# Optimization experiments

Hardware: AMD Instinct MI355X
Metric: run time of the kernel (lower is better)

Reference implementation:

```python
import jax, jax.numpy as jnp
import numpy as np

N = 100000      # nodes
E = 1600000     # edges (avg degree 16)
IN = 128        # in_channels
H = 128         # hidden_channels
OUT = 64        # out_channels
NHID = 3        # num_layers (hidden->hidden SAGE convs)


def _lin(k, fan_out, fan_in):
    s = 1.0 / np.sqrt(fan_in)
    return jax.random.uniform(k, (fan_out, fan_in), jnp.float32, -s, s)


def setup_inputs() -> dict:
    key = jax.random.key(0)
    ks = jax.random.split(key, 12)
    x = jax.random.normal(ks[0], (N, IN), dtype=jnp.float32)
    edge_index = jax.random.randint(ks[1], (2, E), 0, N, dtype=jnp.int32)
    # inProj Linear(IN -> H)
    Wp = _lin(ks[2], H, IN)
    bp = jnp.zeros((H,), jnp.float32)
    # 3 hidden SAGEConv(H -> H): lin_l (with bias) on aggregated neighbors, lin_r (no bias) on root
    Wl_h = jnp.stack([_lin(jax.random.fold_in(ks[3], i), H, H) for i in range(NHID)])
    bl_h = jnp.zeros((NHID, H), jnp.float32)
    Wr_h = jnp.stack([_lin(jax.random.fold_in(ks[4], i), H, H) for i in range(NHID)])
    # output SAGEConv(H -> OUT)
    Wl_o = _lin(ks[5], OUT, H)
    bl_o = jnp.zeros((OUT,), jnp.float32)
    Wr_o = _lin(ks[6], OUT, H)
    return {"x": x, "edge_index": edge_index, "Wp": Wp, "bp": bp,
            "Wl_h": Wl_h, "bl_h": bl_h, "Wr_h": Wr_h,
            "Wl_o": Wl_o, "bl_o": bl_o, "Wr_o": Wr_o}


def reference(x, edge_index, Wp, bp, Wl_h, bl_h, Wr_h, Wl_o, bl_o, Wr_o):
    src, dst = edge_index[0], edge_index[1]
    ones = jnp.ones((E,), x.dtype)
    deg = jax.ops.segment_sum(ones, dst, num_segments=N)           # [N]
    inv_deg = (1.0 / jnp.maximum(deg, 1.0))[:, None]               # [N,1]

    def sage(h, Wl, bl, Wr):
        # mean aggregation of source features onto destinations (irregular gather+scatter)
        s = jax.ops.segment_sum(h[src], dst, num_segments=N)       # [N,d]
        mean = s * inv_deg
        return mean @ Wl.T + bl + h @ Wr.T

    h = x @ Wp.T + bp
    inp = h
    h = jax.nn.relu(h)
    for i in range(NHID):
        h = sage(h, Wl_h[i], bl_h[i], Wr_h[i])
        h = jax.nn.relu(h)                                          # dropout is identity in eval
        h = h + 0.2 * inp
    h = sage(h, Wl_o, bl_o, Wr_o)
    return jax.nn.log_softmax(h, axis=-1)
```

## Files before the change

### kernel.cpp

```cpp
#include <hip/hip_runtime.h>
#include <math.h>

#define N_NODES 100000
#define N_EDGES 1600000
#define NBUK 391
#define PCHUNK 8192
#define NPBLK 196
#define AGG_BLOCKS 12504

typedef unsigned short u16;
typedef unsigned char u8;
typedef __bf16 bf16x8 __attribute__((ext_vector_type(8)));
typedef float f32x4 __attribute__((ext_vector_type(4)));
typedef float f32x2 __attribute__((ext_vector_type(2)));

#define OFF_RP      0u
#define OFF_INVDEG  400016u
#define OFF_BHIST   800016u
#define OFF_BBASE   801600u
#define OFF_GCUR    803200u
#define OFF_PCTR    804800u
#define OFF_PAIRS   805056u
#define OFF_COL     13605056u
#define OFF_PACK    20005056u
#define OFF_INP     20267200u
#define OFF_H       45867200u
#define OFF_H8A     71467200u
#define OFF_H8B     84267200u
#define OFF_GL      97067200u
#define OFF_GR      109867200u
#define OFF_MEAN    122667200u
#define WS_NEEDED   148267200u

#define PK_WP   0
#define PK_WL   16384
#define PK_WR   65536
#define PK_WLO  114688
#define PK_WRO  122880

__device__ __forceinline__ float bfl(unsigned u) {
  union { unsigned i; float f; } v; v.i = u << 16; return v.f;
}
__device__ __forceinline__ float bfh(unsigned u) {
  union { unsigned i; float f; } v; v.i = u & 0xFFFF0000u; return v.f;
}
__device__ __forceinline__ u16 f2b(float f) {
  union { float f; unsigned i; } v; v.f = f;
  unsigned r = (v.i + 0x7FFFu + ((v.i >> 16) & 1u)) >> 16;
  return (u16)r;
}

__global__ __launch_bounds__(256) void pack_weights_k(
    const float* __restrict__ Wp, const float* __restrict__ Wl,
    const float* __restrict__ Wr, const float* __restrict__ Wlo,
    const float* __restrict__ Wro, u16* __restrict__ P) {
  int t = blockIdx.x * 256 + threadIdx.x;
  if (t >= 16384) return;
  const float* W; u16* dst; int j; int NT;
  if (t < 2048)        { W = Wp;                    dst = P + PK_WP;                j = t;                 NT = 8; }
  else if (t < 8192)   { int m = (t - 2048) >> 11;  j = (t - 2048) & 2047;
                         W = Wl + (m << 14);        dst = P + PK_WL + (m << 14);    NT = 8; }
  else if (t < 14336)  { int m = (t - 8192) >> 11;  j = (t - 8192) & 2047;
                         W = Wr + (m << 14);        dst = P + PK_WR + (m << 14);    NT = 8; }
  else if (t < 15360)  { j = t - 14336;             W = Wlo;  dst = P + PK_WLO;     NT = 4; }
  else                 { j = t - 15360;             W = Wro;  dst = P + PK_WRO;     NT = 4; }
  int lane = j & 63;
  int nt, kt;
  if (NT == 8) { nt = (j >> 6) & 7; kt = j >> 9; }
  else         { nt = (j >> 6) & 3; kt = j >> 8; }
  int n  = nt * 16 + (lane & 15);
  int k0 = kt * 32 + ((lane >> 4) << 3);
  const float* s = W + n * 128 + k0;
  ushort4 lo = make_ushort4(f2b(s[0]), f2b(s[1]), f2b(s[2]), f2b(s[3]));
  ushort4 hi = make_ushort4(f2b(s[4]), f2b(s[5]), f2b(s[6]), f2b(s[7]));
  *(ushort4*)(dst + j * 8)     = lo;
  *(ushort4*)(dst + j * 8 + 4) = hi;
}

__global__ __launch_bounds__(256) void bhist_k(const int* __restrict__ dst,
                                               int* __restrict__ bhist) {
  __shared__ int lc[NBUK];
  int t = threadIdx.x;
  for (int i = t; i < NBUK; i += 256) lc[i] = 0;
  __syncthreads();
  int base = blockIdx.x * 4096;
#pragma unroll
  for (int r = 0; r < 16; r++) {
    int i = base + r * 256 + t;
    if (i < N_EDGES) atomicAdd(&lc[dst[i] >> 8], 1);
  }
  __syncthreads();
  for (int i = t; i < NBUK; i += 256)
    if (lc[i]) atomicAdd(&bhist[i], lc[i]);
}

__global__ __launch_bounds__(512) void bscan_k(const int* __restrict__ bhist,
                                               int* __restrict__ bbase,
                                               int* __restrict__ gcur,
                                               int* __restrict__ rp) {
  __shared__ int s[512];
  int t = threadIdx.x;
  int v = (t < NBUK) ? bhist[t] : 0;
  s[t] = v;
  __syncthreads();
  for (int off = 1; off < 512; off <<= 1) {
    int u = (t >= off) ? s[t - off] : 0;
    __syncthreads();
    s[t] += u;
    __syncthreads();
  }
  if (t < NBUK) { int e = s[t] - v; bbase[t] = e; gcur[t] = e; }
  if (t == NBUK - 1) { bbase[NBUK] = s[t]; rp[N_NODES] = s[t]; }
}

__global__ __launch_bounds__(256) void part_k(const int* __restrict__ src,
                                              const int* __restrict__ dst,
                                              int* __restrict__ gcur,
                                              uint2* __restrict__ pairs) {
  __shared__ int lcnt[NBUK + 1];
  __shared__ int lofs[512];
  __shared__ int cur[NBUK];
  __shared__ int gslot[NBUK];
  __shared__ uint2 stag[PCHUNK];
  int t = threadIdx.x;
  for (int i = t; i < NBUK + 1; i += 256) lcnt[i] = 0;
  __syncthreads();
  int base = blockIdx.x * PCHUNK;
#pragma unroll
  for (int r = 0; r < PCHUNK / 256; r++) {
    int i = base + r * 256 + t;
    if (i < N_EDGES) atomicAdd(&lcnt[dst[i] >> 8], 1);
  }
  __syncthreads();
  {
    int e1 = t + 256;
    lofs[t]  = (t  <= NBUK) ? lcnt[t]  : 0;
    lofs[e1] = (e1 <= NBUK) ? lcnt[e1] : 0;
    __syncthreads();
    for (int off = 1; off < 512; off <<= 1) {
      int a0 = (t  >= off) ? lofs[t  - off] : 0;
      int a1 = (e1 >= off) ? lofs[e1 - off] : 0;
      __syncthreads();
      lofs[t] += a0; lofs[e1] += a1;
      __syncthreads();
    }
    int o0 = lofs[t]  - ((t  <= NBUK) ? lcnt[t]  : 0);
    int o1 = lofs[e1] - ((e1 <= NBUK) ? lcnt[e1] : 0);
    __syncthreads();
    lofs[t] = o0; lofs[e1] = o1;
    __syncthreads();
  }
  for (int i = t; i < NBUK; i += 256) cur[i] = lofs[i];
  __syncthreads();
#pragma unroll
  for (int r = 0; r < PCHUNK / 256; r++) {
    int i = base + r * 256 + t;
    if (i < N_EDGES) {
      int d = dst[i];
      int slot = atomicAdd(&cur[d >> 8], 1);
      stag[slot] = make_uint2((unsigned)src[i], (unsigned)d);
    }
  }
  __syncthreads();
  for (int i = t; i < NBUK; i += 256)
    if (lcnt[i]) gslot[i] = atomicAdd(&gcur[i], lcnt[i]);
  __syncthreads();
  int total = lofs[NBUK];
  for (int p = t; p < total; p += 256) {
    uint2 pr = stag[p];
    int b = (int)(pr.y >> 8);
    pairs[gslot[b] + (p - lofs[b])] = pr;
  }
}

__global__ __launch_bounds__(256) void csr_k(const uint2* __restrict__ pairs,
                                             const int* __restrict__ bbase,
                                             int* __restrict__ rp,
                                             float* __restrict__ invdeg,
                                             int* __restrict__ col) {
  __shared__ int cnt[256];
  __shared__ int scn[256];
  __shared__ int cur[256];
  int b = blockIdx.x, t = threadIdx.x;
  int lo = bbase[b], hi = bbase[b + 1];
  cnt[t] = 0;
  __syncthreads();
  for (int p = lo + t; p < hi; p += 256)
    atomicAdd(&cnt[pairs[p].y & 255], 1);
  __syncthreads();
  int c = cnt[t];
  scn[t] = c;
  __syncthreads();
  for (int off = 1; off < 256; off <<= 1) {
    int v = (t >= off) ? scn[t - off] : 0;
    __syncthreads();
    scn[t] += v;
    __syncthreads();
  }
  int excl = scn[t] - c;
  int node = (b << 8) + t;
  if (node < N_NODES) {
    rp[node] = lo + excl;
    invdeg[node] = 1.0f / (float)(c > 1 ? c : 1);
  }
  cur[t] = lo + excl;
  __syncthreads();
  for (int p = lo + t; p < hi; p += 256) {
    uint2 pr = pairs[p];
    int slot = atomicAdd(&cur[pr.y & 255], 1);
    col[slot] = (int)pr.x;
  }
}

__global__ __launch_bounds__(256) void aggregate_plane_k(
    const u8* __restrict__ h8, const int* __restrict__ rp,
    const int* __restrict__ col, const float* __restrict__ invdeg,
    u16* __restrict__ mean) {
  int b = blockIdx.x;
  int plane = (b & 7) >> 1;
  int idx = ((b >> 3) << 1) + (b & 1);
  if (idx >= 3125) return;
  int tid = threadIdx.x;
  int grp = tid >> 3, lane8 = tid & 7;
  int node = idx * 32 + grp;
  const u8* hp = h8 + (size_t)plane * (N_NODES * 32) + lane8 * 4;
  u16* mp = mean + (size_t)plane * (N_NODES * 32);
  int beg = rp[node], end = rp[node + 1];
  float a0 = 0.f, a1 = 0.f, a2 = 0.f, a3 = 0.f;
  int j = beg;
  for (; j + 3 < end; j += 4) {
    int s0 = col[j], s1 = col[j + 1], s2 = col[j + 2], s3 = col[j + 3];
    unsigned v0 = *(const unsigned*)(hp + (size_t)s0 * 32);
    unsigned v1 = *(const unsigned*)(hp + (size_t)s1 * 32);
    unsigned v2 = *(const unsigned*)(hp + (size_t)s2 * 32);
    unsigned v3 = *(const unsigned*)(hp + (size_t)s3 * 32);
    f32x2 p0 = __builtin_amdgcn_cvt_pk_f32_fp8(v0, false);
    f32x2 p1 = __builtin_amdgcn_cvt_pk_f32_fp8(v0, true);
    f32x2 p2 = __builtin_amdgcn_cvt_pk_f32_fp8(v1, false);
    f32x2 p3 = __builtin_amdgcn_cvt_pk_f32_fp8(v1, true);
    f32x2 p4 = __builtin_amdgcn_cvt_pk_f32_fp8(v2, false);
    f32x2 p5 = __builtin_amdgcn_cvt_pk_f32_fp8(v2, true);
    f32x2 p6 = __builtin_amdgcn_cvt_pk_f32_fp8(v3, false);
    f32x2 p7 = __builtin_amdgcn_cvt_pk_f32_fp8(v3, true);
    a0 += (p0[0] + p2[0]) + (p4[0] + p6[0]);
    a1 += (p0[1] + p2[1]) + (p4[1] + p6[1]);
    a2 += (p1[0] + p3[0]) + (p5[0] + p7[0]);
    a3 += (p1[1] + p3[1]) + (p5[1] + p7[1]);
  }
  for (; j < end; j++) {
    unsigned v0 = *(const unsigned*)(hp + (size_t)col[j] * 32);
    f32x2 p0 = __builtin_amdgcn_cvt_pk_f32_fp8(v0, false);
    f32x2 p1 = __builtin_amdgcn_cvt_pk_f32_fp8(v0, true);
    a0 += p0[0]; a1 += p0[1]; a2 += p1[0]; a3 += p1[1];
  }
  float wd = invdeg[node];
  *(ushort4*)(mp + (size_t)node * 32 + lane8 * 4) =
      make_ushort4(f2b(a0 * wd), f2b(a1 * wd), f2b(a2 * wd), f2b(a3 * wd));
}

__global__ __launch_bounds__(256) void out_gather_k(
    const u16* __restrict__ gl, const int* __restrict__ rp,
    const int* __restrict__ col, const float* __restrict__ invdeg,
    float* __restrict__ partial) {
  int b = blockIdx.x;
  int plane = (b & 7) >> 1;
  int idx = ((b >> 3) << 1) + (b & 1);
  if (idx >= 3125) return;
  int tid = threadIdx.x;
  int grp = tid >> 3, lane8 = tid & 7;
  int node = idx * 32 + grp;
  const u16* gp = gl + (size_t)plane * (N_NODES * 16) + lane8 * 2;
  int beg = rp[node], end = rp[node + 1];
  float a0 = 0.f, a1 = 0.f;
  int j = beg;
  for (; j + 3 < end; j += 4) {
    int s0 = col[j], s1 = col[j + 1], s2 = col[j + 2], s3 = col[j + 3];
    unsigned v0 = *(const unsigned*)(gp + (size_t)s0 * 16);
    unsigned v1 = *(const unsigned*)(gp + (size_t)s1 * 16);
    unsigned v2 = *(const unsigned*)(gp + (size_t)s2 * 16);
    unsigned v3 = *(const unsigned*)(gp + (size_t)s3 * 16);
    a0 += (bfl(v0) + bfl(v1)) + (bfl(v2) + bfl(v3));
    a1 += (bfh(v0) + bfh(v1)) + (bfh(v2) + bfh(v3));
  }
  for (; j < end; j++) {
    unsigned v0 = *(const unsigned*)(gp + (size_t)col[j] * 16);
    a0 += bfl(v0); a1 += bfh(v0);
  }
  float wd = invdeg[node];
  *(float2*)(partial + (size_t)node * 64 + plane * 16 + lane8 * 2) =
      make_float2(a0 * wd, a1 * wd);
}

__global__ __launch_bounds__(256) void out_softmax_k(
    const float* __restrict__ partial, const u16* __restrict__ gr,
    const float* __restrict__ blo, float* __restrict__ outp) {
  int node = blockIdx.x * 8 + (threadIdx.x >> 5);
  int lane = threadIdx.x & 31;
  if (node >= N_NODES) return;
  float2 pz = *(const float2*)(partial + (size_t)node * 64 + lane * 2);
  unsigned g = *(const unsigned*)(gr + (size_t)node * 64 + lane * 2);
  float z0 = pz.x + bfl(g) + blo[lane * 2];
  float z1 = pz.y + bfh(g) + blo[lane * 2 + 1];
  float mx = fmaxf(z0, z1);
#pragma unroll
  for (int off = 16; off >= 1; off >>= 1) mx = fmaxf(mx, __shfl_xor(mx, off, 32));
  float s = __expf(z0 - mx) + __expf(z1 - mx);
#pragma unroll
  for (int off = 16; off >= 1; off >>= 1) s += __shfl_xor(s, off, 32);
  float ro = mx + __logf(s);
  float2 o = make_float2(z0 - ro, z1 - ro);
  *(float2*)(outp + (size_t)node * 64 + lane * 2) = o;
}

__global__ __launch_bounds__(256) void inproj_mfma_k(
    const float* __restrict__ X, const u16* __restrict__ P,
    const float* __restrict__ bias,
    u16* __restrict__ inp, u16* __restrict__ hout, u8* __restrict__ h8out, int M) {
  __shared__ float zb[64 * 132];
  int tid = threadIdx.x;
  int w = tid >> 6, lane = tid & 63;
  int quad = lane >> 4, l15 = lane & 15;
  int m0 = blockIdx.x * 64;
  int rowa = m0 + w * 16 + l15; if (rowa > M - 1) rowa = M - 1;
  f32x4 acc[8] = {};
#pragma unroll
  for (int kt = 0; kt < 4; kt++) {
    const float* xr = X + (long)rowa * 128 + kt * 32 + quad * 8;
    float4 p0 = *(const float4*)xr;
    float4 p1 = *(const float4*)(xr + 4);
    union { ushort4 u4[2]; bf16x8 v; } fa;
    fa.u4[0] = make_ushort4(f2b(p0.x), f2b(p0.y), f2b(p0.z), f2b(p0.w));
    fa.u4[1] = make_ushort4(f2b(p1.x), f2b(p1.y), f2b(p1.z), f2b(p1.w));
    const u16* pb = P + ((kt * 8) * 64 + lane) * 8;
#pragma unroll
    for (int nt = 0; nt < 8; nt++) {
      bf16x8 bf = *(const bf16x8*)(pb + nt * 512);
      acc[nt] = __builtin_amdgcn_mfma_f32_16x16x32_bf16(fa.v, bf, acc[nt], 0, 0, 0);
    }
  }
#pragma unroll
  for (int nt = 0; nt < 8; nt++) {
    int c = nt * 16 + l15;
    float b = bias[c];
#pragma unroll
    for (int r = 0; r < 4; r++)
      zb[(w * 16 + quad * 4 + r) * 132 + c] = acc[nt][r] + b;
  }
  __syncthreads();
  int r = lane >> 2, seg = lane & 3;
  long grow = m0 + w * 16 + r;
  if (grow < M) {
    const float* zrow = &zb[(w * 16 + r) * 132 + seg * 32];
    u16* ip = inp + grow * 128 + seg * 32;
    u16* hp = hout + grow * 128 + seg * 32;
    u8*  qp = h8out + (size_t)seg * (N_NODES * 32) + grow * 32;
#pragma unroll
    for (int b = 0; b < 4; b++) {
      float zv[8];
      *(float4*)&zv[0] = *(const float4*)(zrow + b * 8);
      *(float4*)&zv[4] = *(const float4*)(zrow + b * 8 + 4);
      float rv[8];
#pragma unroll
      for (int jj = 0; jj < 8; jj++) rv[jj] = fmaxf(zv[jj], 0.f);
      *(ushort4*)(ip + b * 8)     = make_ushort4(f2b(zv[0]), f2b(zv[1]), f2b(zv[2]), f2b(zv[3]));
      *(ushort4*)(ip + b * 8 + 4) = make_ushort4(f2b(zv[4]), f2b(zv[5]), f2b(zv[6]), f2b(zv[7]));
      *(ushort4*)(hp + b * 8)     = make_ushort4(f2b(rv[0]), f2b(rv[1]), f2b(rv[2]), f2b(rv[3]));
      *(ushort4*)(hp + b * 8 + 4) = make_ushort4(f2b(rv[4]), f2b(rv[5]), f2b(rv[6]), f2b(rv[7]));
      unsigned q0 = 0, q1 = 0;
      q0 = __builtin_amdgcn_cvt_pk_fp8_f32(rv[0], rv[1], q0, false);
      q0 = __builtin_amdgcn_cvt_pk_fp8_f32(rv[2], rv[3], q0, true);
      q1 = __builtin_amdgcn_cvt_pk_fp8_f32(rv[4], rv[5], q1, false);
      q1 = __builtin_amdgcn_cvt_pk_fp8_f32(rv[6], rv[7], q1, true);
      *(uint2*)(qp + b * 8) = make_uint2(q0, q1);
    }
  }
}

__global__ __launch_bounds__(256) void sage_mfma8_k(
    const u16* __restrict__ A0, const u16* __restrict__ P0,
    const u16* __restrict__ A1, const u16* __restrict__ P1,
    const float* __restrict__ bias, const u16* __restrict__ inp,
    u16* __restrict__ outp, u8* __restrict__ h8out, int M) {
  __shared__ float zb[64 * 132];
  int tid = threadIdx.x;
  int w = tid >> 6, lane = tid & 63;
  int quad = lane >> 4, l15 = lane & 15;
  int m0 = blockIdx.x * 64;
  int rowa = m0 + w * 16 + l15; if (rowa > M - 1) rowa = M - 1;
  f32x4 acc[8] = {};
#pragma unroll
  for (int kt = 0; kt < 4; kt++) {
    bf16x8 am = *(const bf16x8*)(A0 + (size_t)kt * (N_NODES * 32) + (size_t)rowa * 32 + quad * 8);
    bf16x8 ar = *(const bf16x8*)(A1 + (long)rowa * 128 + kt * 32 + quad * 8);
    const u16* pl = P0 + ((kt * 8) * 64 + lane) * 8;
    const u16* pr = P1 + ((kt * 8) * 64 + lane) * 8;
#pragma unroll
    for (int nt = 0; nt < 8; nt++) {
      bf16x8 b0 = *(const bf16x8*)(pl + nt * 512);
      bf16x8 b1 = *(const bf16x8*)(pr + nt * 512);
      acc[nt] = __builtin_amdgcn_mfma_f32_16x16x32_bf16(am, b0, acc[nt], 0, 0, 0);
      acc[nt] = __builtin_amdgcn_mfma_f32_16x16x32_bf16(ar, b1, acc[nt], 0, 0, 0);
    }
  }
#pragma unroll
  for (int nt = 0; nt < 8; nt++) {
    int c = nt * 16 + l15;
    float b = bias[c];
#pragma unroll
    for (int r = 0; r < 4; r++)
      zb[(w * 16 + quad * 4 + r) * 132 + c] = fmaxf(acc[nt][r] + b, 0.f);
  }
  __syncthreads();
  int r = lane >> 2, seg = lane & 3;
  long grow = m0 + w * 16 + r;
  if (grow < M) {
    const float* zrow = &zb[(w * 16 + r) * 132 + seg * 32];
    const u16* ip = inp + grow * 128 + seg * 32;
    u16* op = outp + grow * 128 + seg * 32;
#pragma unroll
    for (int b = 0; b < 4; b++) {
      float zv[8];
      *(float4*)&zv[0] = *(const float4*)(zrow + b * 8);
      *(float4*)&zv[4] = *(const float4*)(zrow + b * 8 + 4);
      uint2 iv0 = *(const uint2*)(ip + b * 8);
      uint2 iv1 = *(const uint2*)(ip + b * 8 + 4);
      float fv[8];
      fv[0] = zv[0] + 0.2f * bfl(iv0.x); fv[1] = zv[1] + 0.2f * bfh(iv0.x);
      fv[2] = zv[2] + 0.2f * bfl(iv0.y); fv[3] = zv[3] + 0.2f * bfh(iv0.y);
      fv[4] = zv[4] + 0.2f * bfl(iv1.x); fv[5] = zv[5] + 0.2f * bfh(iv1.x);
      fv[6] = zv[6] + 0.2f * bfl(iv1.y); fv[7] = zv[7] + 0.2f * bfh(iv1.y);
      *(ushort4*)(op + b * 8)     = make_ushort4(f2b(fv[0]), f2b(fv[1]), f2b(fv[2]), f2b(fv[3]));
      *(ushort4*)(op + b * 8 + 4) = make_ushort4(f2b(fv[4]), f2b(fv[5]), f2b(fv[6]), f2b(fv[7]));
      if (h8out) {
        unsigned q0 = 0, q1 = 0;
        q0 = __builtin_amdgcn_cvt_pk_fp8_f32(fv[0], fv[1], q0, false);
        q0 = __builtin_amdgcn_cvt_pk_fp8_f32(fv[2], fv[3], q0, true);
        q1 = __builtin_amdgcn_cvt_pk_fp8_f32(fv[4], fv[5], q1, false);
        q1 = __builtin_amdgcn_cvt_pk_fp8_f32(fv[6], fv[7], q1, true);
        *(uint2*)(h8out + (size_t)seg * (N_NODES * 32) + grow * 32 + b * 8) = make_uint2(q0, q1);
      }
    }
  }
}

__global__ __launch_bounds__(256) void out_proj_k(
    const u16* __restrict__ A, const u16* __restrict__ PLO,
    const u16* __restrict__ PRO, u16* __restrict__ gl, u16* __restrict__ gr, int M) {
  __shared__ float zb[64 * 132];
  int tid = threadIdx.x;
  int w = tid >> 6, lane = tid & 63;
  int quad = lane >> 4, l15 = lane & 15;
  int m0 = blockIdx.x * 64;
  int rowa = m0 + w * 16 + l15; if (rowa > M - 1) rowa = M - 1;
  f32x4 acc[8] = {};
#pragma unroll
  for (int kt = 0; kt < 4; kt++) {
    bf16x8 af = *(const bf16x8*)(A + (long)rowa * 128 + kt * 32 + quad * 8);
#pragma unroll
    for (int nt = 0; nt < 4; nt++) {
      bf16x8 b0 = *(const bf16x8*)(PLO + ((kt * 4 + nt) * 64 + lane) * 8);
      bf16x8 b1 = *(const bf16x8*)(PRO + ((kt * 4 + nt) * 64 + lane) * 8);
      acc[nt]     = __builtin_amdgcn_mfma_f32_16x16x32_bf16(af, b0, acc[nt], 0, 0, 0);
      acc[4 + nt] = __builtin_amdgcn_mfma_f32_16x16x32_bf16(af, b1, acc[4 + nt], 0, 0, 0);
    }
  }
#pragma unroll
  for (int nt = 0; nt < 4; nt++) {
    int c = nt * 16 + l15;
#pragma unroll
    for (int r = 0; r < 4; r++) {
      zb[(w * 16 + quad * 4 + r) * 132 + c]      = acc[nt][r];
      zb[(w * 16 + quad * 4 + r) * 132 + 64 + c] = acc[4 + nt][r];
    }
  }
  __syncthreads();
  int r = lane >> 2, seg = lane & 3;
  long grow = m0 + w * 16 + r;
  if (grow < M) {
    const float* zrow = &zb[(w * 16 + r) * 132 + seg * 32];
#pragma unroll
    for (int b = 0; b < 4; b++) {
      float zv[8];
      *(float4*)&zv[0] = *(const float4*)(zrow + b * 8);
      *(float4*)&zv[4] = *(const float4*)(zrow + b * 8 + 4);
      u16* dp;
      if (seg < 2) {
        int plane = seg * 2 + (b >> 1);
        dp = gl + (size_t)plane * (N_NODES * 16) + grow * 16 + (b & 1) * 8;
      } else {
        dp = gr + grow * 64 + (seg - 2) * 32 + b * 8;
      }
      *(ushort4*)(dp)     = make_ushort4(f2b(zv[0]), f2b(zv[1]), f2b(zv[2]), f2b(zv[3]));
      *(ushort4*)(dp + 4) = make_ushort4(f2b(zv[4]), f2b(zv[5]), f2b(zv[6]), f2b(zv[7]));
    }
  }
}

extern "C" void kernel_launch(void* const* d_in, const int* in_sizes, int n_in,
                              void* d_out, int out_size, void* d_ws, size_t ws_size,
                              hipStream_t stream) {
  if (ws_size < (size_t)WS_NEEDED) return;
  const float* x   = (const float*)d_in[0];
  const int*   ei  = (const int*)d_in[1];
  const float* Wp  = (const float*)d_in[2];
  const float* bp  = (const float*)d_in[3];
  const float* Wl  = (const float*)d_in[4];
  const float* bl  = (const float*)d_in[5];
  const float* Wr  = (const float*)d_in[6];
  const float* Wlo = (const float*)d_in[7];
  const float* blo = (const float*)d_in[8];
  const float* Wro = (const float*)d_in[9];
  float* out = (float*)d_out;
  char* ws = (char*)d_ws;
  int*   rp     = (int*)(ws + OFF_RP);
  float* invdeg = (float*)(ws + OFF_INVDEG);
  int*   bhist  = (int*)(ws + OFF_BHIST);
  int*   bbase  = (int*)(ws + OFF_BBASE);
  int*   gcur   = (int*)(ws + OFF_GCUR);
  uint2* pairs  = (uint2*)(ws + OFF_PAIRS);
  int*   col    = (int*)(ws + OFF_COL);
  u16*   pack   = (u16*)(ws + OFF_PACK);
  u16*   inp    = (u16*)(ws + OFF_INP);
  u16*   h      = (u16*)(ws + OFF_H);
  u8*    h8a    = (u8*)(ws + OFF_H8A);
  u8*    h8b    = (u8*)(ws + OFF_H8B);
  u16*   gl     = (u16*)(ws + OFF_GL);
  u16*   gr     = (u16*)(ws + OFF_GR);
  u16*   mean   = (u16*)(ws + OFF_MEAN);
  float* partial = (float*)(ws + OFF_MEAN);
  const int* srcv = ei;
  const int* dstv = ei + N_EDGES;

  hipMemsetAsync(ws + OFF_BHIST, 0, OFF_PAIRS - OFF_BHIST, stream);
  pack_weights_k<<<64, 256, 0, stream>>>(Wp, Wl, Wr, Wlo, Wro, pack);
  bhist_k<<<391, 256, 0, stream>>>(dstv, bhist);
  bscan_k<<<1, 512, 0, stream>>>(bhist, bbase, gcur, rp);
  part_k<<<NPBLK, 256, 0, stream>>>(srcv, dstv, gcur, pairs);
  csr_k<<<NBUK, 256, 0, stream>>>(pairs, bbase, rp, invdeg, col);

  int gblk = (N_NODES + 63) / 64;
  int fblk = (N_NODES + 7) / 8;

  inproj_mfma_k<<<gblk, 256, 0, stream>>>(x, pack + PK_WP, bp, inp, h, h8a, N_NODES);

  aggregate_plane_k<<<AGG_BLOCKS, 256, 0, stream>>>(h8a, rp, col, invdeg, mean);
  sage_mfma8_k<<<gblk, 256, 0, stream>>>(mean, pack + PK_WL, h, pack + PK_WR,
                                         bl, inp, h, h8b, N_NODES);
  aggregate_plane_k<<<AGG_BLOCKS, 256, 0, stream>>>(h8b, rp, col, invdeg, mean);
  sage_mfma8_k<<<gblk, 256, 0, stream>>>(mean, pack + PK_WL + 16384, h, pack + PK_WR + 16384,
                                         bl + 128, inp, h, h8a, N_NODES);
  aggregate_plane_k<<<AGG_BLOCKS, 256, 0, stream>>>(h8a, rp, col, invdeg, mean);
  sage_mfma8_k<<<gblk, 256, 0, stream>>>(mean, pack + PK_WL + 32768, h, pack + PK_WR + 32768,
                                         bl + 256, inp, h, (u8*)nullptr, N_NODES);

  out_proj_k<<<gblk, 256, 0, stream>>>(h, pack + PK_WLO, pack + PK_WRO, gl, gr, N_NODES);
  out_gather_k<<<AGG_BLOCKS, 256, 0, stream>>>(gl, rp, col, invdeg, partial);
  out_softmax_k<<<fblk, 256, 0, stream>>>(partial, gr, blo, out);
}
```

Baseline: 546.5 us.

## Switch gather features from column-plane layout to row-major with cooperative index loads

Feature buffers (fp8 hidden, bf16 mean, out-projection gl) move from four column planes to row-major rows. Each gather kernel now handles full 128-byte or 128-byte rows per node with one 16-byte load per lane, in one pass instead of four plane passes. Neighbor indices are loaded cooperatively by the 8 lanes and broadcast with shuffles. This cuts repeated rp/col reads and launches four times fewer blocks, at the cost of more registers per thread and less L2 locality per plane.

```diff
diff --git a/kernel.cpp b/kernel.cpp
--- a/kernel.cpp
+++ b/kernel.cpp
@@ -6,7 +6,7 @@
 #define NBUK 391
 #define PCHUNK 8192
 #define NPBLK 196
-#define AGG_BLOCKS 12504
+#define GBLK32 3125
 
 typedef unsigned short u16;
 typedef unsigned char u8;
@@ -212,83 +212,82 @@
   }
 }
 
-__global__ __launch_bounds__(256) void aggregate_plane_k(
+__global__ __launch_bounds__(256) void aggregate_row_k(
     const u8* __restrict__ h8, const int* __restrict__ rp,
     const int* __restrict__ col, const float* __restrict__ invdeg,
     u16* __restrict__ mean) {
-  int b = blockIdx.x;
-  int plane = (b & 7) >> 1;
-  int idx = ((b >> 3) << 1) + (b & 1);
-  if (idx >= 3125) return;
   int tid = threadIdx.x;
   int grp = tid >> 3, lane8 = tid & 7;
-  int node = idx * 32 + grp;
-  const u8* hp = h8 + (size_t)plane * (N_NODES * 32) + lane8 * 4;
-  u16* mp = mean + (size_t)plane * (N_NODES * 32);
+  int node = blockIdx.x * 32 + grp;
   int beg = rp[node], end = rp[node + 1];
-  float a0 = 0.f, a1 = 0.f, a2 = 0.f, a3 = 0.f;
-  int j = beg;
-  for (; j + 3 < end; j += 4) {
-    int s0 = col[j], s1 = col[j + 1], s2 = col[j + 2], s3 = col[j + 3];
-    unsigned v0 = *(const unsigned*)(hp + (size_t)s0 * 32);
-    unsigned v1 = *(const unsigned*)(hp + (size_t)s1 * 32);
-    unsigned v2 = *(const unsigned*)(hp + (size_t)s2 * 32);
-    unsigned v3 = *(const unsigned*)(hp + (size_t)s3 * 32);
-    f32x2 p0 = __builtin_amdgcn_cvt_pk_f32_fp8(v0, false);
-    f32x2 p1 = __builtin_amdgcn_cvt_pk_f32_fp8(v0, true);
-    f32x2 p2 = __builtin_amdgcn_cvt_pk_f32_fp8(v1, false);
-    f32x2 p3 = __builtin_amdgcn_cvt_pk_f32_fp8(v1, true);
-    f32x2 p4 = __builtin_amdgcn_cvt_pk_f32_fp8(v2, false);
-    f32x2 p5 = __builtin_amdgcn_cvt_pk_f32_fp8(v2, true);
-    f32x2 p6 = __builtin_amdgcn_cvt_pk_f32_fp8(v3, false);
-    f32x2 p7 = __builtin_amdgcn_cvt_pk_f32_fp8(v3, true);
-    a0 += (p0[0] + p2[0]) + (p4[0] + p6[0]);
-    a1 += (p0[1] + p2[1]) + (p4[1] + p6[1]);
-    a2 += (p1[0] + p3[0]) + (p5[0] + p7[0]);
-    a3 += (p1[1] + p3[1]) + (p5[1] + p7[1]);
-  }
-  for (; j < end; j++) {
-    unsigned v0 = *(const unsigned*)(hp + (size_t)col[j] * 32);
-    f32x2 p0 = __builtin_amdgcn_cvt_pk_f32_fp8(v0, false);
-    f32x2 p1 = __builtin_amdgcn_cvt_pk_f32_fp8(v0, true);
-    a0 += p0[0]; a1 += p0[1]; a2 += p1[0]; a3 += p1[1];
+  const u8* hp = h8 + lane8 * 16;
+  float a[16];
+#pragma unroll
+  for (int i = 0; i < 16; i++) a[i] = 0.f;
+  for (int j = beg; j < end; j += 8) {
+    int ci = 0;
+    if (j + lane8 < end) ci = col[j + lane8];
+    int cnt = end - j;
+#pragma unroll
+    for (int e = 0; e < 8; e++) {
+      if (e < cnt) {
+        int s = __shfl(ci, e, 8);
+        uint4 v = *(const uint4*)(hp + (size_t)s * 128);
+        f32x2 p0 = __builtin_amdgcn_cvt_pk_f32_fp8(v.x, false);
+        f32x2 p1 = __builtin_amdgcn_cvt_pk_f32_fp8(v.x, true);
+        f32x2 p2 = __builtin_amdgcn_cvt_pk_f32_fp8(v.y, false);
+        f32x2 p3 = __builtin_amdgcn_cvt_pk_f32_fp8(v.y, true);
+        f32x2 p4 = __builtin_amdgcn_cvt_pk_f32_fp8(v.z, false);
+        f32x2 p5 = __builtin_amdgcn_cvt_pk_f32_fp8(v.z, true);
+        f32x2 p6 = __builtin_amdgcn_cvt_pk_f32_fp8(v.w, false);
+        f32x2 p7 = __builtin_amdgcn_cvt_pk_f32_fp8(v.w, true);
+        a[0]  += p0[0]; a[1]  += p0[1]; a[2]  += p1[0]; a[3]  += p1[1];
+        a[4]  += p2[0]; a[5]  += p2[1]; a[6]  += p3[0]; a[7]  += p3[1];
+        a[8]  += p4[0]; a[9]  += p4[1]; a[10] += p5[0]; a[11] += p5[1];
+        a[12] += p6[0]; a[13] += p6[1]; a[14] += p7[0]; a[15] += p7[1];
+      }
+    }
   }
   float wd = invdeg[node];
-  *(ushort4*)(mp + (size_t)node * 32 + lane8 * 4) =
-      make_ushort4(f2b(a0 * wd), f2b(a1 * wd), f2b(a2 * wd), f2b(a3 * wd));
+  u16* mp = mean + (size_t)node * 128 + lane8 * 16;
+  *(ushort4*)(mp)      = make_ushort4(f2b(a[0]*wd),  f2b(a[1]*wd),  f2b(a[2]*wd),  f2b(a[3]*wd));
+  *(ushort4*)(mp + 4)  = make_ushort4(f2b(a[4]*wd),  f2b(a[5]*wd),  f2b(a[6]*wd),  f2b(a[7]*wd));
+  *(ushort4*)(mp + 8)  = make_ushort4(f2b(a[8]*wd),  f2b(a[9]*wd),  f2b(a[10]*wd), f2b(a[11]*wd));
+  *(ushort4*)(mp + 12) = make_ushort4(f2b(a[12]*wd), f2b(a[13]*wd), f2b(a[14]*wd), f2b(a[15]*wd));
 }
 
 __global__ __launch_bounds__(256) void out_gather_k(
     const u16* __restrict__ gl, const int* __restrict__ rp,
     const int* __restrict__ col, const float* __restrict__ invdeg,
     float* __restrict__ partial) {
-  int b = blockIdx.x;
-  int plane = (b & 7) >> 1;
-  int idx = ((b >> 3) << 1) + (b & 1);
-  if (idx >= 3125) return;
   int tid = threadIdx.x;
   int grp = tid >> 3, lane8 = tid & 7;
-  int node = idx * 32 + grp;
-  const u16* gp = gl + (size_t)plane * (N_NODES * 16) + lane8 * 2;
+  int node = blockIdx.x * 32 + grp;
   int beg = rp[node], end = rp[node + 1];
-  float a0 = 0.f, a1 = 0.f;
-  int j = beg;
-  for (; j + 3 < end; j += 4) {
-    int s0 = col[j], s1 = col[j + 1], s2 = col[j + 2], s3 = col[j + 3];
-    unsigned v0 = *(const unsigned*)(gp + (size_t)s0 * 16);
-    unsigned v1 = *(const unsigned*)(gp + (size_t)s1 * 16);
-    unsigned v2 = *(const unsigned*)(gp + (size_t)s2 * 16);
-    unsigned v3 = *(const unsigned*)(gp + (size_t)s3 * 16);
-    a0 += (bfl(v0) + bfl(v1)) + (bfl(v2) + bfl(v3));
-    a1 += (bfh(v0) + bfh(v1)) + (bfh(v2) + bfh(v3));
-  }
-  for (; j < end; j++) {
-    unsigned v0 = *(const unsigned*)(gp + (size_t)col[j] * 16);
-    a0 += bfl(v0); a1 += bfh(v0);
+  const u16* gp = gl + lane8 * 8;
+  float a[8];
+#pragma unroll
+  for (int i = 0; i < 8; i++) a[i] = 0.f;
+  for (int j = beg; j < end; j += 8) {
+    int ci = 0;
+    if (j + lane8 < end) ci = col[j + lane8];
+    int cnt = end - j;
+#pragma unroll
+    for (int e = 0; e < 8; e++) {
+      if (e < cnt) {
+        int s = __shfl(ci, e, 8);
+        uint4 v = *(const uint4*)(gp + (size_t)s * 64);
+        a[0] += bfl(v.x); a[1] += bfh(v.x);
+        a[2] += bfl(v.y); a[3] += bfh(v.y);
+        a[4] += bfl(v.z); a[5] += bfh(v.z);
+        a[6] += bfl(v.w); a[7] += bfh(v.w);
+      }
+    }
   }
   float wd = invdeg[node];
-  *(float2*)(partial + (size_t)node * 64 + plane * 16 + lane8 * 2) =
-      make_float2(a0 * wd, a1 * wd);
+  float* pp = partial + (size_t)node * 64 + lane8 * 8;
+  *(float4*)(pp)     = make_float4(a[0]*wd, a[1]*wd, a[2]*wd, a[3]*wd);
+  *(float4*)(pp + 4) = make_float4(a[4]*wd, a[5]*wd, a[6]*wd, a[7]*wd);
 }
 
 __global__ __launch_bounds__(256) void out_softmax_k(
@@ -353,7 +352,7 @@
     const float* zrow = &zb[(w * 16 + r) * 132 + seg * 32];
     u16* ip = inp + grow * 128 + seg * 32;
     u16* hp = hout + grow * 128 + seg * 32;
-    u8*  qp = h8out + (size_t)seg * (N_NODES * 32) + grow * 32;
+    u8*  qp = h8out + grow * 128 + seg * 32;
 #pragma unroll
     for (int b = 0; b < 4; b++) {
       float zv[8];
@@ -390,7 +389,7 @@
   f32x4 acc[8] = {};
 #pragma unroll
   for (int kt = 0; kt < 4; kt++) {
-    bf16x8 am = *(const bf16x8*)(A0 + (size_t)kt * (N_NODES * 32) + (size_t)rowa * 32 + quad * 8);
+    bf16x8 am = *(const bf16x8*)(A0 + (long)rowa * 128 + kt * 32 + quad * 8);
     bf16x8 ar = *(const bf16x8*)(A1 + (long)rowa * 128 + kt * 32 + quad * 8);
     const u16* pl = P0 + ((kt * 8) * 64 + lane) * 8;
     const u16* pr = P1 + ((kt * 8) * 64 + lane) * 8;
@@ -437,7 +436,7 @@
         q0 = __builtin_amdgcn_cvt_pk_fp8_f32(fv[2], fv[3], q0, true);
         q1 = __builtin_amdgcn_cvt_pk_fp8_f32(fv[4], fv[5], q1, false);
         q1 = __builtin_amdgcn_cvt_pk_fp8_f32(fv[6], fv[7], q1, true);
-        *(uint2*)(h8out + (size_t)seg * (N_NODES * 32) + grow * 32 + b * 8) = make_uint2(q0, q1);
+        *(uint2*)(h8out + grow * 128 + seg * 32 + b * 8) = make_uint2(q0, q1);
       }
     }
   }
@@ -478,20 +477,14 @@
   long grow = m0 + w * 16 + r;
   if (grow < M) {
     const float* zrow = &zb[(w * 16 + r) * 132 + seg * 32];
+    u16* dp = (seg < 2) ? (gl + grow * 64 + seg * 32) : (gr + grow * 64 + (seg - 2) * 32);
 #pragma unroll
     for (int b = 0; b < 4; b++) {
       float zv[8];
       *(float4*)&zv[0] = *(const float4*)(zrow + b * 8);
       *(float4*)&zv[4] = *(const float4*)(zrow + b * 8 + 4);
-      u16* dp;
-      if (seg < 2) {
-        int plane = seg * 2 + (b >> 1);
-        dp = gl + (size_t)plane * (N_NODES * 16) + grow * 16 + (b & 1) * 8;
-      } else {
-        dp = gr + grow * 64 + (seg - 2) * 32 + b * 8;
-      }
-      *(ushort4*)(dp)     = make_ushort4(f2b(zv[0]), f2b(zv[1]), f2b(zv[2]), f2b(zv[3]));
-      *(ushort4*)(dp + 4) = make_ushort4(f2b(zv[4]), f2b(zv[5]), f2b(zv[6]), f2b(zv[7]));
+      *(ushort4*)(dp + b * 8)     = make_ushort4(f2b(zv[0]), f2b(zv[1]), f2b(zv[2]), f2b(zv[3]));
+      *(ushort4*)(dp + b * 8 + 4) = make_ushort4(f2b(zv[4]), f2b(zv[5]), f2b(zv[6]), f2b(zv[7]));
     }
   }
 }
@@ -543,17 +536,17 @@
 
   inproj_mfma_k<<<gblk, 256, 0, stream>>>(x, pack + PK_WP, bp, inp, h, h8a, N_NODES);
 
-  aggregate_plane_k<<<AGG_BLOCKS, 256, 0, stream>>>(h8a, rp, col, invdeg, mean);
+  aggregate_row_k<<<GBLK32, 256, 0, stream>>>(h8a, rp, col, invdeg, mean);
   sage_mfma8_k<<<gblk, 256, 0, stream>>>(mean, pack + PK_WL, h, pack + PK_WR,
                                          bl, inp, h, h8b, N_NODES);
-  aggregate_plane_k<<<AGG_BLOCKS, 256, 0, stream>>>(h8b, rp, col, invdeg, mean);
+  aggregate_row_k<<<GBLK32, 256, 0, stream>>>(h8b, rp, col, invdeg, mean);
   sage_mfma8_k<<<gblk, 256, 0, stream>>>(mean, pack + PK_WL + 16384, h, pack + PK_WR + 16384,
                                          bl + 128, inp, h, h8a, N_NODES);
-  aggregate_plane_k<<<AGG_BLOCKS, 256, 0, stream>>>(h8a, rp, col, invdeg, mean);
+  aggregate_row_k<<<GBLK32, 256, 0, stream>>>(h8a, rp, col, invdeg, mean);
   sage_mfma8_k<<<gblk, 256, 0, stream>>>(mean, pack + PK_WL + 32768, h, pack + PK_WR + 32768,
                                          bl + 256, inp, h, (u8*)nullptr, N_NODES);
 
   out_proj_k<<<gblk, 256, 0, stream>>>(h, pack + PK_WLO, pack + PK_WRO, gl, gr, N_NODES);
-  out_gather_k<<<AGG_BLOCKS, 256, 0, stream>>>(gl, rp, col, invdeg, partial);
+  out_gather_k<<<GBLK32, 256, 0, stream>>>(gl, rp, col, invdeg, partial);
   out_softmax_k<<<fblk, 256, 0, stream>>>(partial, gr, blo, out);
 }
```

Result: no change. 556.4 us (+1.8%).
